# Optimization experiments

Hardware: AMD Instinct MI355X
Metric: run time of the kernel (lower is better)

## Reference

```python
import jax, jax.numpy as jnp
import numpy as np

B = 2
H = 256; Wd = 256; C = 128; S = 16        # image dims, channels, split_size
G = (H // S) * (Wd // S)                  # 256 heads (spatial groups)
N = S * S                                 # 256 patches per head
CI = C // 2                               # 64 channels per branch (gmlp input)
EI = 6                                    # inner gMLP expansion (MabGmlpBlock default e)
F1 = CI * EI                              # 384 = LocallyConnected expansion width
HF = F1 // 2                              # 192 = u/v split width
EPS = 1e-3                                # keras LayerNormalization default epsilon


def layer_norm(x, g, b):
    m = jnp.mean(x, axis=-1, keepdims=True)
    v = jnp.var(x, axis=-1, keepdims=True)
    return (x - m) * jax.lax.rsqrt(v + EPS) * g + b


def make_blocks(x):
    # 'B (H b1) (W b2) C -> B (H W) (b1 b2) C'
    b_, _, _, c_ = x.shape
    x = x.reshape(b_, H // S, S, Wd // S, S, c_)
    return x.transpose(0, 1, 3, 2, 4, 5).reshape(b_, G, N, c_)


def recon_blocks(x):
    # 'B (H W) (b1 b2) C -> B (H b1) (W b2) C'
    b_, _, _, c_ = x.shape
    x = x.reshape(b_, H // S, Wd // S, S, S, c_)
    return x.transpose(0, 1, 3, 2, 4, 5).reshape(b_, H, Wd, c_)


def recon_grids(x):
    # 'B (H W) (d1 d2) C -> B (d1 H) (d2 W) C'
    b_, _, _, c_ = x.shape
    x = x.reshape(b_, H // S, Wd // S, S, S, c_)
    return x.transpose(0, 3, 1, 4, 2, 5).reshape(b_, H, Wd, c_)


def gmlp(x, ln2_g, ln2_b, W1, b1, ln3_g, ln3_b, Wsgu, bsgu, W2, b2):
    # x: [B, G, N, CI]; all heads share weights -> batched einsum over (B, G)
    y = layer_norm(x, ln2_g, ln2_b)
    # LocallyConnected1D kernel_size=1: per-patch distinct weight [N, CI, F1]
    y = jax.nn.gelu(jnp.einsum('bgnc,ncf->bgnf', y, W1) + b1, approximate=False)
    u, v = jnp.split(y, 2, axis=-1)                      # [B,G,N,HF] each
    u = layer_norm(u, ln3_g, ln3_b)
    u = jnp.swapaxes(u, -1, -2)                          # [B,G,HF,N]
    # spatial gating: per-channel distinct [N->N] mixing, bias init ones
    u = jnp.einsum('bgcn,cnm->bgcm', u, Wsgu) + bsgu
    u = jnp.swapaxes(u, -1, -2)                          # [B,G,N,HF]
    return jnp.einsum('bgnc,ncf->bgnf', u * v, W2) + b2 + x


def setup_inputs() -> dict:
    key = jax.random.key(0)
    ks = jax.random.split(key, 8)
    x = jax.random.normal(ks[0], (B, H, Wd, C), jnp.float32)
    W_proj = jax.random.normal(ks[1], (C, C), jnp.float32) / np.sqrt(C).astype(np.float32)
    b_proj = jnp.zeros((C,), jnp.float32)
    W1 = jax.random.normal(ks[2], (N, CI, F1), jnp.float32) / np.sqrt(CI).astype(np.float32)
    b1 = jnp.zeros((N, F1), jnp.float32)
    Wsgu = jax.random.normal(ks[3], (HF, N, N), jnp.float32) * 0.001  # truncated_normal(0.001) approx
    bsgu = jnp.ones((HF, N), jnp.float32)                             # bias_initializer=ones
    W2 = jax.random.normal(ks[4], (N, HF, CI), jnp.float32) / np.sqrt(HF).astype(np.float32)
    b2 = jnp.zeros((N, CI), jnp.float32)
    return {
        'x': x,
        'ln1_g': jnp.ones((C,), jnp.float32), 'ln1_b': jnp.zeros((C,), jnp.float32),
        'W_proj': W_proj, 'b_proj': b_proj,
        'ln2_g': jnp.ones((CI,), jnp.float32), 'ln2_b': jnp.zeros((CI,), jnp.float32),
        'W1': W1, 'b1': b1,
        'ln3_g': jnp.ones((HF,), jnp.float32), 'ln3_b': jnp.zeros((HF,), jnp.float32),
        'Wsgu': Wsgu, 'bsgu': bsgu,
        'W2': W2, 'b2': b2,
    }


def reference(x, ln1_g, ln1_b, W_proj, b_proj, ln2_g, ln2_b, W1, b1,
              ln3_g, ln3_b, Wsgu, bsgu, W2, b2):
    y = layer_norm(x, ln1_g, ln1_b)
    y = jax.nn.gelu(y @ W_proj + b_proj, approximate=False)   # Dense(c*e), e=1
    local, glob = jnp.split(y, 2, axis=-1)                    # [B,H,W,CI] each
    g_args = (ln2_g, ln2_b, W1, b1, ln3_g, ln3_b, Wsgu, bsgu, W2, b2)
    local = recon_grids(gmlp(make_blocks(local), *g_args))    # multi-axis: block in, grid out
    glob = recon_blocks(gmlp(make_blocks(glob), *g_args))
    out = jnp.concatenate([local, glob], axis=-1) + x
    return out, glob
```

## Files before the change

kernel.cpp:

```cpp
#include <hip/hip_runtime.h>


typedef unsigned int uint_t;
typedef unsigned short us_t;
typedef __attribute__((ext_vector_type(8))) short bf16x8;
typedef __attribute__((ext_vector_type(4))) float f32x4;

#define EPSF 1e-3f

__device__ __forceinline__ float b2f(us_t h){ return __uint_as_float(((uint_t)h) << 16); }
__device__ __forceinline__ float lo2f(uint_t u){ return __uint_as_float(u << 16); }
__device__ __forceinline__ float hi2f(uint_t u){ return __uint_as_float(u & 0xFFFF0000u); }
__device__ __forceinline__ us_t f2b(float f){
  uint_t u = __float_as_uint(f);
  uint_t r = (u + 0x7FFFu + ((u >> 16) & 1u)) >> 16;
  return (us_t)r;
}
__device__ __forceinline__ uint_t pack2(float a, float b){
  return (uint_t)f2b(a) | ((uint_t)f2b(b) << 16);
}
__device__ __forceinline__ float gelu_f(float v){
  return 0.5f*v*(1.f + erff(v*0.7071067811865475f));
}

__global__ __launch_bounds__(256) void wprep(const float* __restrict__ Wsgu,
                                             const float* __restrict__ Wp,
                                             us_t* __restrict__ WT,
                                             us_t* __restrict__ WpT){
  __shared__ __align__(16) us_t ls[128*136];
  int t = threadIdx.x;
  if (blockIdx.x == 768){
    #pragma unroll
    for (int i = 0; i < 16; i++){
      int idx = (i*256 + t)*4;
      int row = idx >> 7, col = idx & 127;
      float4 w = *(const float4*)(Wp + idx);
      ls[(col+0)*136 + row] = f2b(w.x);
      ls[(col+1)*136 + row] = f2b(w.y);
      ls[(col+2)*136 + row] = f2b(w.z);
      ls[(col+3)*136 + row] = f2b(w.w);
    }
    __syncthreads();
    #pragma unroll
    for (int i = 0; i < 8; i++){
      int chunk = i*256 + t;
      int o = chunk >> 4, i0 = (chunk & 15) << 3;
      *(uint4*)(WpT + o*128 + i0) = *(const uint4*)&ls[o*136 + i0];
    }
    return;
  }
  int c = blockIdx.x >> 2, kt = blockIdx.x & 3;
  const float* src = Wsgu + ((size_t)c*256 + kt*64)*256;
  #pragma unroll
  for (int i = 0; i < 16; i++){
    int chunk = i*256 + t;
    int kk = chunk >> 6, mm = (chunk & 63) << 2;
    float4 w = *(const float4*)(src + kk*256 + mm);
    *(uint2*)&ls[kk*264 + mm] = make_uint2(pack2(w.x,w.y), pack2(w.z,w.w));
  }
  __syncthreads();
  #pragma unroll
  for (int i = 0; i < 8; i++){
    int chunk = i*256 + t;
    int m = chunk >> 3, kk0 = (chunk & 7) << 3;
    const us_t* sp = &ls[kk0*264 + m];
    uint4 o;
    o.x = (uint_t)sp[0]     | ((uint_t)sp[264]   << 16);
    o.y = (uint_t)sp[2*264] | ((uint_t)sp[3*264] << 16);
    o.z = (uint_t)sp[4*264] | ((uint_t)sp[5*264] << 16);
    o.w = (uint_t)sp[6*264] | ((uint_t)sp[7*264] << 16);
    *(uint4*)(WT + ((size_t)c*256 + m)*256 + kt*64 + kk0) = o;
  }
}

__global__ __launch_bounds__(256) void w1t(const float* __restrict__ W1,
                                           us_t* __restrict__ W1T){
  __shared__ __align__(16) us_t ls[64*392];
  int t = threadIdx.x;
  const float* src = W1 + (size_t)blockIdx.x * 24576;
  #pragma unroll
  for (int i = 0; i < 24; i++){
    int idx = (i*256 + t)*4;
    int ci = idx / 384, f = idx - ci*384;
    float4 w = *(const float4*)(src + idx);
    *(uint2*)&ls[ci*392 + f] = make_uint2(pack2(w.x,w.y), pack2(w.z,w.w));
  }
  __syncthreads();
  us_t* dstb = W1T + (size_t)blockIdx.x * 24576;
  #pragma unroll
  for (int i = 0; i < 12; i++){
    int chunk = i*256 + t;
    int f = chunk >> 3, ci0 = (chunk & 7) << 3;
    const us_t* sp = &ls[ci0*392 + f];
    uint4 o;
    o.x = (uint_t)sp[0]     | ((uint_t)sp[392]   << 16);
    o.y = (uint_t)sp[2*392] | ((uint_t)sp[3*392] << 16);
    o.z = (uint_t)sp[4*392] | ((uint_t)sp[5*392] << 16);
    o.w = (uint_t)sp[6*392] | ((uint_t)sp[7*392] << 16);
    *(uint4*)(dstb + f*64 + ci0) = o;
  }
}

__global__ __launch_bounds__(256) void k1_ln_proj(
    const float* __restrict__ x, const float* __restrict__ g1, const float* __restrict__ b1l,
    const us_t* __restrict__ WpT, const float* __restrict__ bp, us_t* __restrict__ xin)
{
  __shared__ __align__(16) us_t As[128*136];
  __shared__ __align__(16) us_t Ws[128*136];
  __shared__ float gs[128], bs[128];
  int t = threadIdx.x;
  int p0 = blockIdx.x * 128;
  int lane = t & 63, wv = t >> 6;

  if (t < 128){ gs[t] = g1[t]; bs[t] = b1l[t]; }
  #pragma unroll
  for (int i = 0; i < 8; i++){
    int chunk = i*256 + t;
    int row = chunk >> 4, k0 = (chunk & 15) << 3;
    *(uint4*)&Ws[row*136 + k0] = *(const uint4*)(WpT + row*128 + k0);
  }
  int pl = t >> 1, half = t & 1;
  const float* xr = x + (size_t)(p0 + pl)*128 + half*64;
  float xv[64];
  float s = 0.f, q = 0.f;
  #pragma unroll
  for (int i = 0; i < 16; i++){
    float4 d = *(const float4*)(xr + i*4);
    xv[i*4+0] = d.x; xv[i*4+1] = d.y; xv[i*4+2] = d.z; xv[i*4+3] = d.w;
    s += d.x + d.y + d.z + d.w;
    q += d.x*d.x + d.y*d.y + d.z*d.z + d.w*d.w;
  }
  s += __shfl_xor(s, 1, 64);
  q += __shfl_xor(q, 1, 64);
  float m = s*(1.f/128.f);
  float rstd = rsqrtf(q*(1.f/128.f) - m*m + EPSF);
  __syncthreads();
  {
    int c0 = half << 6;
    us_t* dst = &As[pl*136 + c0];
    #pragma unroll
    for (int jj = 0; jj < 8; jj++){
      float y[8];
      #pragma unroll
      for (int k = 0; k < 8; k++){
        int idx = jj*8 + k;
        y[k] = (xv[idx] - m)*rstd*gs[c0 + idx] + bs[c0 + idx];
      }
      uint4 o;
      o.x = pack2(y[0], y[1]);
      o.y = pack2(y[2], y[3]);
      o.z = pack2(y[4], y[5]);
      o.w = pack2(y[6], y[7]);
      *(uint4*)&dst[jj*8] = o;
    }
  }
  __syncthreads();
  int wm0 = (wv >> 1) * 64, wn0 = (wv & 1) * 64;
  int fr = lane & 15, fq = lane >> 4;
  f32x4 acc[4][4] = {};
  #pragma unroll
  for (int sstep = 0; sstep < 4; sstep++){
    int kb = sstep*32 + fq*8;
    bf16x8 a[4], b[4];
    #pragma unroll
    for (int mi = 0; mi < 4; mi++)
      a[mi] = *(const bf16x8*)&Ws[(wm0 + mi*16 + fr)*136 + kb];
    #pragma unroll
    for (int ni = 0; ni < 4; ni++)
      b[ni] = *(const bf16x8*)&As[(wn0 + ni*16 + fr)*136 + kb];
    #pragma unroll
    for (int mi = 0; mi < 4; mi++)
      #pragma unroll
      for (int ni = 0; ni < 4; ni++)
        acc[mi][ni] = __builtin_amdgcn_mfma_f32_16x16x32_bf16(a[mi], b[ni], acc[mi][ni], 0, 0, 0);
  }
  #pragma unroll
  for (int mi = 0; mi < 4; mi++){
    int ch0 = wm0 + mi*16 + fq*4;
    float4 bb = *(const float4*)(bp + ch0);
    int branch = ch0 >> 6, c = ch0 & 63;
    #pragma unroll
    for (int ni = 0; ni < 4; ni++){
      int p = p0 + wn0 + ni*16 + fr;
      int b_ = p >> 16, rem = p & 65535, h = rem >> 8, w = rem & 255;
      int g = ((h >> 4) << 4) | (w >> 4);
      int nn = ((h & 15) << 4) | (w & 15);
      float v0 = gelu_f(acc[mi][ni][0] + bb.x);
      float v1 = gelu_f(acc[mi][ni][1] + bb.y);
      float v2 = gelu_f(acc[mi][ni][2] + bb.z);
      float v3 = gelu_f(acc[mi][ni][3] + bb.w);
      size_t row = (size_t)branch*512 + (size_t)b_*256 + g;
      *(uint2*)(xin + (row*256 + nn)*64 + c) = make_uint2(pack2(v0,v1), pack2(v2,v3));
    }
  }
}

__global__ __launch_bounds__(256) void k2_e1(
    const us_t* __restrict__ xin, const us_t* __restrict__ W1T,
    const float* __restrict__ g2, const float* __restrict__ b2l,
    const float* __restrict__ b1v,
    const float* __restrict__ g3, const float* __restrict__ b3l,
    us_t* __restrict__ u_ln, us_t* __restrict__ vout, int r_base)
{
  __shared__ __align__(16) us_t Bs[192*72];
  __shared__ __align__(16) us_t As[128*72];
  __shared__ __align__(16) float b1s[192];
  __shared__ __align__(16) float g3s[192];
  __shared__ __align__(16) float b3s[192];
  __shared__ __align__(16) float g2s[64];
  __shared__ __align__(16) float b2s[64];
  int t = threadIdx.x;
  int n = blockIdx.x >> 1, uv = blockIdx.x & 1;
  int lane = t & 63, wv = t >> 6;
  int fr = lane & 15, fq = lane >> 4;

  const us_t* wsrc = W1T + (size_t)n*24576 + uv*12288;
  #pragma unroll
  for (int i = 0; i < 6; i++){
    int chunk = i*256 + t;
    int f = chunk >> 3, ci0 = (chunk & 7) << 3;
    *(uint4*)&Bs[f*72 + ci0] = *(const uint4*)(wsrc + chunk*8);
  }
  if (t < 48)        *(float4*)&b1s[t*4]       = *(const float4*)(b1v + n*384 + uv*192 + t*4);
  else if (t < 96)   *(float4*)&g3s[(t-48)*4]  = *(const float4*)(g3  + (t-48)*4);
  else if (t < 144)  *(float4*)&b3s[(t-96)*4]  = *(const float4*)(b3l + (t-96)*4);
  else if (t < 160)  *(float4*)&g2s[(t-144)*4] = *(const float4*)(g2  + (t-144)*4);
  else if (t < 176)  *(float4*)&b2s[(t-160)*4] = *(const float4*)(b2l + (t-160)*4);

  int rr = t >> 1, half = t & 1;
  const us_t* xsrc = xin + ((size_t)(r_base + rr)*256 + n)*64 + half*32;
  uint4 d0 = *(const uint4*)(xsrc);
  uint4 d1 = *(const uint4*)(xsrc + 8);
  uint4 d2 = *(const uint4*)(xsrc + 16);
  uint4 d3 = *(const uint4*)(xsrc + 24);
  float xv[32];
  {
    uint4 dd[4] = {d0, d1, d2, d3};
    #pragma unroll
    for (int j = 0; j < 4; j++){
      xv[j*8+0]=lo2f(dd[j].x); xv[j*8+1]=hi2f(dd[j].x);
      xv[j*8+2]=lo2f(dd[j].y); xv[j*8+3]=hi2f(dd[j].y);
      xv[j*8+4]=lo2f(dd[j].z); xv[j*8+5]=hi2f(dd[j].z);
      xv[j*8+6]=lo2f(dd[j].w); xv[j*8+7]=hi2f(dd[j].w);
    }
  }
  float s = 0.f, q = 0.f;
  #pragma unroll
  for (int j = 0; j < 32; j++){ s += xv[j]; q += xv[j]*xv[j]; }
  s += __shfl_xor(s, 1, 64);
  q += __shfl_xor(q, 1, 64);
  float m = s*(1.f/64.f);
  float rstd = rsqrtf(q*(1.f/64.f) - m*m + EPSF);
  __syncthreads();
  {
    int cb = half*32;
    us_t* dst = &As[rr*72 + cb];
    #pragma unroll
    for (int jj = 0; jj < 4; jj++){
      float y[8];
      #pragma unroll
      for (int k = 0; k < 8; k++){
        int idx = cb + jj*8 + k;
        y[k] = (xv[jj*8+k] - m)*rstd*g2s[idx] + b2s[idx];
      }
      uint4 o;
      o.x = pack2(y[0], y[1]);
      o.y = pack2(y[2], y[3]);
      o.z = pack2(y[4], y[5]);
      o.w = pack2(y[6], y[7]);
      *(uint4*)&dst[jj*8] = o;
    }
  }
  __syncthreads();

  int wr0 = wv*32;
  f32x4 acc[2][12] = {};
  #pragma unroll
  for (int ks = 0; ks < 2; ks++){
    int kb = ks*32 + fq*8;
    bf16x8 a0 = *(const bf16x8*)&As[(wr0 + fr)*72 + kb];
    bf16x8 a1 = *(const bf16x8*)&As[(wr0 + 16 + fr)*72 + kb];
    #pragma unroll
    for (int ni = 0; ni < 12; ni++){
      bf16x8 b = *(const bf16x8*)&Bs[(ni*16 + fr)*72 + kb];
      acc[0][ni] = __builtin_amdgcn_mfma_f32_16x16x32_bf16(a0, b, acc[0][ni], 0, 0, 0);
      acc[1][ni] = __builtin_amdgcn_mfma_f32_16x16x32_bf16(a1, b, acc[1][ni], 0, 0, 0);
    }
  }

  float bsv[12];
  #pragma unroll
  for (int ni = 0; ni < 12; ni++) bsv[ni] = b1s[ni*16 + fr];
  if (uv == 0){
    float g3v[12], b3v[12];
    #pragma unroll
    for (int ni = 0; ni < 12; ni++){ g3v[ni] = g3s[ni*16+fr]; b3v[ni] = b3s[ni*16+fr]; }
    #pragma unroll
    for (int mi = 0; mi < 2; mi++){
      #pragma unroll
      for (int i = 0; i < 4; i++){
        int r = wr0 + mi*16 + fq*4 + i;
        float y[12];
        float ss = 0.f, qq = 0.f;
        #pragma unroll
        for (int ni = 0; ni < 12; ni++){
          float yv = gelu_f(acc[mi][ni][i] + bsv[ni]);
          y[ni] = yv; ss += yv; qq += yv*yv;
        }
        #pragma unroll
        for (int off = 8; off; off >>= 1){ ss += __shfl_xor(ss, off, 64); qq += __shfl_xor(qq, off, 64); }
        float mm = ss*(1.f/192.f);
        float rs = rsqrtf(qq*(1.f/192.f) - mm*mm + EPSF);
        us_t* dst = u_ln + ((size_t)r*256 + n)*192 + fr;
        #pragma unroll
        for (int ni = 0; ni < 12; ni++)
          dst[ni*16] = f2b((y[ni]-mm)*rs*g3v[ni] + b3v[ni]);
      }
    }
  } else {
    #pragma unroll
    for (int mi = 0; mi < 2; mi++){
      #pragma unroll
      for (int i = 0; i < 4; i++){
        int r = wr0 + mi*16 + fq*4 + i;
        us_t* dst = vout + ((size_t)r*256 + n)*192 + fr;
        #pragma unroll
        for (int ni = 0; ni < 12; ni++)
          dst[ni*16] = f2b(gelu_f(acc[mi][ni][i] + bsv[ni]));
      }
    }
  }
}

__global__ __launch_bounds__(256) void t1_transpose(const us_t* __restrict__ u_ln, us_t* __restrict__ uT){
  __shared__ us_t ls[128*194];
  int t = threadIdx.x;
  int r = blockIdx.x >> 1, n0 = (blockIdx.x & 1) << 7;
  #pragma unroll
  for (int i = 0; i < 12; i++){
    int chunk = i*256 + t;
    int nn = chunk/24, c0 = (chunk - nn*24)*8;
    uint4 d = *(const uint4*)(u_ln + ((size_t)r*256 + n0 + nn)*192 + c0);
    us_t* dst = &ls[nn*194 + c0];
    dst[0] = (us_t)d.x; dst[1] = (us_t)(d.x>>16);
    dst[2] = (us_t)d.y; dst[3] = (us_t)(d.y>>16);
    dst[4] = (us_t)d.z; dst[5] = (us_t)(d.z>>16);
    dst[6] = (us_t)d.w; dst[7] = (us_t)(d.w>>16);
  }
  __syncthreads();
  #pragma unroll
  for (int i = 0; i < 12; i++){
    int chunk = i*256 + t;
    int c = chunk >> 4, nn0 = (chunk & 15) << 3;
    const us_t* sp = &ls[nn0*194 + c];
    uint4 o;
    o.x = (uint_t)sp[0]     | ((uint_t)sp[194]   << 16);
    o.y = (uint_t)sp[2*194] | ((uint_t)sp[3*194] << 16);
    o.z = (uint_t)sp[4*194] | ((uint_t)sp[5*194] << 16);
    o.w = (uint_t)sp[6*194] | ((uint_t)sp[7*194] << 16);
    *(uint4*)(uT + ((size_t)c*128 + r)*256 + n0 + nn0) = o;
  }
}

__global__ __launch_bounds__(256) void k3_sgu_mfma(
    const us_t* __restrict__ uT, const us_t* __restrict__ WT,
    const float* __restrict__ bsgu, us_t* __restrict__ sT)
{
  __shared__ __align__(16) us_t As[128*72];
  __shared__ __align__(16) us_t Bs[128*72];
  int t = threadIdx.x;
  int c = blockIdx.x >> 1, mt = blockIdx.x & 1;
  int lane = t & 63, wv = t >> 6;
  int wr0 = (wv >> 1) * 64, wm0 = (wv & 1) * 64;
  int fr = lane & 15, fq = lane >> 4;
  f32x4 acc[4][4] = {};

  const us_t* aSrc = uT + (size_t)c*128*256;
  const us_t* bSrc = WT + ((size_t)(c*256 + mt*128))*256;

  for (int ks = 0; ks < 256; ks += 64){
    #pragma unroll
    for (int i = 0; i < 4; i++){
      int chunk = i*256 + t;
      int rr = chunk >> 3, kk = (chunk & 7) << 3;
      *(uint4*)&As[rr*72 + kk] = *(const uint4*)(aSrc + rr*256 + ks + kk);
      *(uint4*)&Bs[rr*72 + kk] = *(const uint4*)(bSrc + rr*256 + ks + kk);
    }
    __syncthreads();
    #pragma unroll
    for (int s = 0; s < 2; s++){
      int kb = s*32 + fq*8;
      bf16x8 a[4], b[4];
      #pragma unroll
      for (int mi = 0; mi < 4; mi++)
        a[mi] = *(const bf16x8*)&As[(wr0 + mi*16 + fr)*72 + kb];
      #pragma unroll
      for (int ni = 0; ni < 4; ni++)
        b[ni] = *(const bf16x8*)&Bs[(wm0 + ni*16 + fr)*72 + kb];
      #pragma unroll
      for (int mi = 0; mi < 4; mi++)
        #pragma unroll
        for (int ni = 0; ni < 4; ni++)
          acc[mi][ni] = __builtin_amdgcn_mfma_f32_16x16x32_bf16(a[mi], b[ni], acc[mi][ni], 0, 0, 0);
    }
    __syncthreads();
  }
  float bsv[4];
  #pragma unroll
  for (int ni = 0; ni < 4; ni++)
    bsv[ni] = bsgu[c*256 + mt*128 + wm0 + ni*16 + fr];
  #pragma unroll
  for (int mi = 0; mi < 4; mi++){
    #pragma unroll
    for (int i = 0; i < 4; i++){
      int r = wr0 + mi*16 + fq*4 + i;
      us_t* dst = sT + ((size_t)c*128 + r)*256 + mt*128 + wm0 + fr;
      #pragma unroll
      for (int ni = 0; ni < 4; ni++)
        dst[ni*16] = f2b(acc[mi][ni][i] + bsv[ni]);
    }
  }
}

__global__ __launch_bounds__(256) void t2_mul(
    const us_t* __restrict__ sT, const us_t* __restrict__ v, us_t* __restrict__ tout)
{
  __shared__ us_t ls[192*130];
  int t = threadIdx.x;
  int r = blockIdx.x >> 1, m0 = (blockIdx.x & 1) << 7;
  #pragma unroll
  for (int i = 0; i < 12; i++){
    int chunk = i*256 + t;
    int c = chunk >> 4, mm0 = (chunk & 15) << 3;
    uint4 d = *(const uint4*)(sT + ((size_t)c*128 + r)*256 + m0 + mm0);
    us_t* dst = &ls[c*130 + mm0];
    dst[0] = (us_t)d.x; dst[1] = (us_t)(d.x>>16);
    dst[2] = (us_t)d.y; dst[3] = (us_t)(d.y>>16);
    dst[4] = (us_t)d.z; dst[5] = (us_t)(d.z>>16);
    dst[6] = (us_t)d.w; dst[7] = (us_t)(d.w>>16);
  }
  __syncthreads();
  #pragma unroll
  for (int i = 0; i < 12; i++){
    int chunk = i*256 + t;
    int mm = chunk/24, c0 = (chunk - mm*24)*8;
    size_t gidx = ((size_t)r*256 + m0 + mm)*192 + c0;
    uint4 vv = *(const uint4*)(v + gidx);
    const us_t* sp = &ls[c0*130 + mm];
    uint4 o;
    o.x = pack2(b2f(sp[0])*lo2f(vv.x),     b2f(sp[130])*hi2f(vv.x));
    o.y = pack2(b2f(sp[2*130])*lo2f(vv.y), b2f(sp[3*130])*hi2f(vv.y));
    o.z = pack2(b2f(sp[4*130])*lo2f(vv.z), b2f(sp[5*130])*hi2f(vv.z));
    o.w = pack2(b2f(sp[6*130])*lo2f(vv.w), b2f(sp[7*130])*hi2f(vv.w));
    *(uint4*)(tout + gidx) = o;
  }
}

__global__ __launch_bounds__(256) void k4_out(
    const us_t* __restrict__ tbuf, const float* __restrict__ W2,
    const float* __restrict__ b2v, const us_t* __restrict__ xin,
    const float* __restrict__ x, float* __restrict__ out0, float* __restrict__ out1,
    int r_base)
{
  __shared__ __align__(16) us_t W2s[192*64];
  __shared__ __align__(16) us_t ts[192*68];
  int t = threadIdx.x;
  int n = blockIdx.x >> 1, rt = blockIdx.x & 1;
  const float* wsrc = W2 + (size_t)n*12288;
  #pragma unroll
  for (int i = 0; i < 12; i++){
    int idx = (i*256 + t)*4;
    float4 w = *(const float4*)(wsrc + idx);
    *(uint2*)&W2s[idx] = make_uint2(pack2(w.x,w.y), pack2(w.z,w.w));
  }
  #pragma unroll
  for (int i = 0; i < 6; i++){
    int chunk = i*256 + t;
    int rr = chunk/24, ff0 = (chunk - rr*24)*8;
    uint4 d = *(const uint4*)(tbuf + ((size_t)(rt*64 + rr)*256 + n)*192 + ff0);
    us_t* dst = &ts[ff0*68 + rr];
    dst[0]    = (us_t)d.x; dst[68]   = (us_t)(d.x>>16);
    dst[2*68] = (us_t)d.y; dst[3*68] = (us_t)(d.y>>16);
    dst[4*68] = (us_t)d.z; dst[5*68] = (us_t)(d.z>>16);
    dst[6*68] = (us_t)d.w; dst[7*68] = (us_t)(d.w>>16);
  }
  __syncthreads();
  int cg = t & 15, rg = t >> 4;
  int c0 = cg*4, rr0 = rg*4;
  float acc[4][4] = {};
  #pragma unroll 4
  for (int f = 0; f < 192; f++){
    uint2 au = *(const uint2*)&ts[f*68 + rr0];
    uint2 wu = *(const uint2*)&W2s[f*64 + c0];
    float a0 = lo2f(au.x), a1 = hi2f(au.x), a2 = lo2f(au.y), a3 = hi2f(au.y);
    float w0 = lo2f(wu.x), w1 = hi2f(wu.x), w2 = lo2f(wu.y), w3 = hi2f(wu.y);
    acc[0][0] += a0*w0; acc[0][1] += a0*w1; acc[0][2] += a0*w2; acc[0][3] += a0*w3;
    acc[1][0] += a1*w0; acc[1][1] += a1*w1; acc[1][2] += a1*w2; acc[1][3] += a1*w3;
    acc[2][0] += a2*w0; acc[2][1] += a2*w1; acc[2][2] += a2*w2; acc[2][3] += a2*w3;
    acc[3][0] += a3*w0; acc[3][1] += a3*w1; acc[3][2] += a3*w2; acc[3][3] += a3*w3;
  }
  float4 bb = *(const float4*)(b2v + n*64 + c0);
  #pragma unroll
  for (int i = 0; i < 4; i++){
    int rl = rt*64 + rr0 + i;
    int r = r_base + rl;
    int branch = r >> 9, bidx = (r >> 8) & 1, g = r & 255;
    uint2 xi = *(const uint2*)(xin + ((size_t)r*256 + n)*64 + c0);
    float v0 = acc[i][0] + bb.x + lo2f(xi.x);
    float v1 = acc[i][1] + bb.y + hi2f(xi.x);
    float v2 = acc[i][2] + bb.z + lo2f(xi.y);
    float v3 = acc[i][3] + bb.w + hi2f(xi.y);
    int h, w;
    if (branch == 0){ h = ((n >> 4) << 4) | (g >> 4); w = ((n & 15) << 4) | (g & 15); }
    else            { h = ((g >> 4) << 4) | (n >> 4); w = ((g & 15) << 4) | (n & 15); }
    size_t base = (size_t)(bidx*256 + h)*256 + w;
    size_t o0idx = base*128 + (branch << 6) + c0;
    float4 xr = *(const float4*)(x + o0idx);
    *(float4*)(out0 + o0idx) = make_float4(v0 + xr.x, v1 + xr.y, v2 + xr.z, v3 + xr.w);
    if (branch){
      *(float4*)(out1 + base*64 + c0) = make_float4(v0, v1, v2, v3);
    }
  }
}

extern "C" void kernel_launch(void* const* d_in, const int* in_sizes, int n_in,
                              void* d_out, int out_size, void* d_ws, size_t ws_size,
                              hipStream_t stream)
{
  (void)in_sizes; (void)n_in; (void)out_size;
  const float* x    = (const float*)d_in[0];
  const float* g1   = (const float*)d_in[1];
  const float* b1l  = (const float*)d_in[2];
  const float* Wp   = (const float*)d_in[3];
  const float* bp   = (const float*)d_in[4];
  const float* g2   = (const float*)d_in[5];
  const float* b2l  = (const float*)d_in[6];
  const float* W1   = (const float*)d_in[7];
  const float* b1v  = (const float*)d_in[8];
  const float* g3   = (const float*)d_in[9];
  const float* b3l  = (const float*)d_in[10];
  const float* Wsgu = (const float*)d_in[11];
  const float* bsgu = (const float*)d_in[12];
  const float* W2   = (const float*)d_in[13];
  const float* b2v  = (const float*)d_in[14];

  float* out0 = (float*)d_out;
  float* out1 = out0 + (size_t)2*256*256*128;

  us_t* ws   = (us_t*)d_ws;
  us_t* xin  = ws;
  us_t* bufA = ws + 16777216;
  us_t* bufV = bufA + 6291456;
  us_t* bufB = bufV + 6291456;
  us_t* WT   = bufB + 6291456;
  us_t* WpT  = WT + 12582912;

  bool dedicated = ws_size >= 109084672ULL;
  us_t* W1T = dedicated ? (WpT + 16384) : bufB;

  wprep      <<<dim3(769),  dim3(256), 0, stream>>>(Wsgu, Wp, WT, WpT);
  if (dedicated)
    w1t      <<<dim3(256),  dim3(256), 0, stream>>>(W1, W1T);
  k1_ln_proj <<<dim3(1024), dim3(256), 0, stream>>>(x, g1, b1l, WpT, bp, xin);
  for (int chunk = 0; chunk < 8; ++chunk){
    int r_base = chunk * 128;
    if (!dedicated)
      w1t       <<<dim3(256),  dim3(256), 0, stream>>>(W1, W1T);
    k2_e1       <<<dim3(512),  dim3(256), 0, stream>>>(xin, W1T, g2, b2l, b1v, g3, b3l, bufA, bufV, r_base);
    t1_transpose<<<dim3(256),  dim3(256), 0, stream>>>(bufA, bufB);
    k3_sgu_mfma <<<dim3(384),  dim3(256), 0, stream>>>(bufB, WT, bsgu, bufA);
    t2_mul      <<<dim3(256),  dim3(256), 0, stream>>>(bufA, bufV, bufB);
    k4_out      <<<dim3(512),  dim3(256), 0, stream>>>(bufB, W2, b2v, xin, x, out0, out1, r_base);
  }
}
```

Measured before the change: 1.050 ms.

## Fuse SGU gating multiply into output kernel and stage k1 stores through LDS

k1's epilogue now writes GELU results into shared memory and then does coalesced 16-byte global stores to the blocked xin layout, replacing scattered 8-byte stores. k3 swaps its MFMA operands so the SGU output comes out in a [c][m][r] layout. The t2_mul kernel is removed and the u*v gating is folded into k4_out's staging load, which saves one kernel launch per chunk and a full round-trip of the intermediate buffer. The cost is that k4 now does scalar 2-byte gathers from st2, which may be poorly coalesced.

```diff
diff --git a/kernel.cpp b/kernel.cpp
--- a/kernel.cpp
+++ b/kernel.cpp
@@ -174,24 +174,34 @@
       for (int ni = 0; ni < 4; ni++)
         acc[mi][ni] = __builtin_amdgcn_mfma_f32_16x16x32_bf16(a[mi], b[ni], acc[mi][ni], 0, 0, 0);
   }
+  __syncthreads();
   #pragma unroll
   for (int mi = 0; mi < 4; mi++){
     int ch0 = wm0 + mi*16 + fq*4;
     float4 bb = *(const float4*)(bp + ch0);
-    int branch = ch0 >> 6, c = ch0 & 63;
     #pragma unroll
     for (int ni = 0; ni < 4; ni++){
-      int p = p0 + wn0 + ni*16 + fr;
-      int b_ = p >> 16, rem = p & 65535, h = rem >> 8, w = rem & 255;
-      int g = ((h >> 4) << 4) | (w >> 4);
-      int nn = ((h & 15) << 4) | (w & 15);
+      int pix = wn0 + ni*16 + fr;
       float v0 = gelu_f(acc[mi][ni][0] + bb.x);
       float v1 = gelu_f(acc[mi][ni][1] + bb.y);
       float v2 = gelu_f(acc[mi][ni][2] + bb.z);
       float v3 = gelu_f(acc[mi][ni][3] + bb.w);
-      size_t row = (size_t)branch*512 + (size_t)b_*256 + g;
-      *(uint2*)(xin + (row*256 + nn)*64 + c) = make_uint2(pack2(v0,v1), pack2(v2,v3));
-    }
+      *(uint2*)&As[pix*136 + ch0] = make_uint2(pack2(v0,v1), pack2(v2,v3));
+    }
+  }
+  __syncthreads();
+  #pragma unroll
+  for (int i = 0; i < 8; i++){
+    int chunk = i*256 + t;
+    int pix = chunk >> 4, cq = chunk & 15;
+    int ch0b = cq*8;
+    int p = p0 + pix;
+    int b_ = p >> 16, rem = p & 65535, h = rem >> 8, w = rem & 255;
+    int g = ((h >> 4) << 4) | (w >> 4);
+    int nn = ((h & 15) << 4) | (w & 15);
+    int branch = ch0b >> 6, c = ch0b & 63;
+    size_t row = (size_t)branch*512 + (size_t)b_*256 + g;
+    *(uint4*)(xin + (row*256 + nn)*64 + c) = *(const uint4*)&As[pix*136 + ch0b];
   }
 }
 
@@ -364,7 +374,7 @@
 
 __global__ __launch_bounds__(256) void k3_sgu_mfma(
     const us_t* __restrict__ uT, const us_t* __restrict__ WT,
-    const float* __restrict__ bsgu, us_t* __restrict__ sT)
+    const float* __restrict__ bsgu, us_t* __restrict__ st2)
 {
   __shared__ __align__(16) us_t As[128*72];
   __shared__ __align__(16) us_t Bs[128*72];
@@ -393,10 +403,10 @@
       bf16x8 a[4], b[4];
       #pragma unroll
       for (int mi = 0; mi < 4; mi++)
-        a[mi] = *(const bf16x8*)&As[(wr0 + mi*16 + fr)*72 + kb];
+        a[mi] = *(const bf16x8*)&Bs[(wm0 + mi*16 + fr)*72 + kb];
       #pragma unroll
       for (int ni = 0; ni < 4; ni++)
-        b[ni] = *(const bf16x8*)&Bs[(wm0 + ni*16 + fr)*72 + kb];
+        b[ni] = *(const bf16x8*)&As[(wr0 + ni*16 + fr)*72 + kb];
       #pragma unroll
       for (int mi = 0; mi < 4; mi++)
         #pragma unroll
@@ -405,59 +415,23 @@
     }
     __syncthreads();
   }
-  float bsv[4];
-  #pragma unroll
-  for (int ni = 0; ni < 4; ni++)
-    bsv[ni] = bsgu[c*256 + mt*128 + wm0 + ni*16 + fr];
   #pragma unroll
   for (int mi = 0; mi < 4; mi++){
     #pragma unroll
     for (int i = 0; i < 4; i++){
-      int r = wr0 + mi*16 + fq*4 + i;
-      us_t* dst = sT + ((size_t)c*128 + r)*256 + mt*128 + wm0 + fr;
+      int mg = mt*128 + wm0 + mi*16 + fq*4 + i;
+      float bias = bsgu[c*256 + mg];
+      us_t* dst = st2 + ((size_t)c*256 + mg)*128 + wr0 + fr;
       #pragma unroll
       for (int ni = 0; ni < 4; ni++)
-        dst[ni*16] = f2b(acc[mi][ni][i] + bsv[ni]);
-    }
-  }
-}
-
-__global__ __launch_bounds__(256) void t2_mul(
-    const us_t* __restrict__ sT, const us_t* __restrict__ v, us_t* __restrict__ tout)
-{
-  __shared__ us_t ls[192*130];
-  int t = threadIdx.x;
-  int r = blockIdx.x >> 1, m0 = (blockIdx.x & 1) << 7;
-  #pragma unroll
-  for (int i = 0; i < 12; i++){
-    int chunk = i*256 + t;
-    int c = chunk >> 4, mm0 = (chunk & 15) << 3;
-    uint4 d = *(const uint4*)(sT + ((size_t)c*128 + r)*256 + m0 + mm0);
-    us_t* dst = &ls[c*130 + mm0];
-    dst[0] = (us_t)d.x; dst[1] = (us_t)(d.x>>16);
-    dst[2] = (us_t)d.y; dst[3] = (us_t)(d.y>>16);
-    dst[4] = (us_t)d.z; dst[5] = (us_t)(d.z>>16);
-    dst[6] = (us_t)d.w; dst[7] = (us_t)(d.w>>16);
-  }
-  __syncthreads();
-  #pragma unroll
-  for (int i = 0; i < 12; i++){
-    int chunk = i*256 + t;
-    int mm = chunk/24, c0 = (chunk - mm*24)*8;
-    size_t gidx = ((size_t)r*256 + m0 + mm)*192 + c0;
-    uint4 vv = *(const uint4*)(v + gidx);
-    const us_t* sp = &ls[c0*130 + mm];
-    uint4 o;
-    o.x = pack2(b2f(sp[0])*lo2f(vv.x),     b2f(sp[130])*hi2f(vv.x));
-    o.y = pack2(b2f(sp[2*130])*lo2f(vv.y), b2f(sp[3*130])*hi2f(vv.y));
-    o.z = pack2(b2f(sp[4*130])*lo2f(vv.z), b2f(sp[5*130])*hi2f(vv.z));
-    o.w = pack2(b2f(sp[6*130])*lo2f(vv.w), b2f(sp[7*130])*hi2f(vv.w));
-    *(uint4*)(tout + gidx) = o;
+        dst[ni*16] = f2b(acc[mi][ni][i] + bias);
+    }
   }
 }
 
 __global__ __launch_bounds__(256) void k4_out(
-    const us_t* __restrict__ tbuf, const float* __restrict__ W2,
+    const us_t* __restrict__ st2, const us_t* __restrict__ v,
+    const float* __restrict__ W2,
     const float* __restrict__ b2v, const us_t* __restrict__ xin,
     const float* __restrict__ x, float* __restrict__ out0, float* __restrict__ out1,
     int r_base)
@@ -477,12 +451,17 @@
   for (int i = 0; i < 6; i++){
     int chunk = i*256 + t;
     int rr = chunk/24, ff0 = (chunk - rr*24)*8;
-    uint4 d = *(const uint4*)(tbuf + ((size_t)(rt*64 + rr)*256 + n)*192 + ff0);
+    int r = rt*64 + rr;
+    uint4 vv = *(const uint4*)(v + ((size_t)r*256 + n)*192 + ff0);
+    float vf[8];
+    vf[0]=lo2f(vv.x); vf[1]=hi2f(vv.x); vf[2]=lo2f(vv.y); vf[3]=hi2f(vv.y);
+    vf[4]=lo2f(vv.z); vf[5]=hi2f(vv.z); vf[6]=lo2f(vv.w); vf[7]=hi2f(vv.w);
     us_t* dst = &ts[ff0*68 + rr];
-    dst[0]    = (us_t)d.x; dst[68]   = (us_t)(d.x>>16);
-    dst[2*68] = (us_t)d.y; dst[3*68] = (us_t)(d.y>>16);
-    dst[4*68] = (us_t)d.z; dst[5*68] = (us_t)(d.z>>16);
-    dst[6*68] = (us_t)d.w; dst[7*68] = (us_t)(d.w>>16);
+    #pragma unroll
+    for (int j = 0; j < 8; j++){
+      us_t sv = st2[((size_t)(ff0 + j)*256 + n)*128 + r];
+      dst[j*68] = f2b(b2f(sv) * vf[j]);
+    }
   }
   __syncthreads();
   int cg = t & 15, rg = t >> 4;
@@ -569,7 +548,6 @@
     k2_e1       <<<dim3(512),  dim3(256), 0, stream>>>(xin, W1T, g2, b2l, b1v, g3, b3l, bufA, bufV, r_base);
     t1_transpose<<<dim3(256),  dim3(256), 0, stream>>>(bufA, bufB);
     k3_sgu_mfma <<<dim3(384),  dim3(256), 0, stream>>>(bufB, WT, bsgu, bufA);
-    t2_mul      <<<dim3(256),  dim3(256), 0, stream>>>(bufA, bufV, bufB);
-    k4_out      <<<dim3(512),  dim3(256), 0, stream>>>(bufB, W2, b2v, xin, x, out0, out1, r_base);
-  }
-}
+    k4_out      <<<dim3(512),  dim3(256), 0, stream>>>(bufA, bufV, W2, b2v, xin, x, out0, out1, r_base);
+  }
+}
```

After: 1.051 ms. No clear change (+0.2%).
